# Kernel tuning notes

Measured on AMD Instinct MI355X. Metric: run time of the kernel, lower is better.

Reference implementation:

```python
import jax, jax.numpy as jnp
import numpy as np

D_STATE = 16
DT_RANK = 6
EPS = 1e-5


def layer_norm(x, w, b):
    mu = jnp.mean(x, axis=-1, keepdims=True)
    var = jnp.mean((x - mu) ** 2, axis=-1, keepdims=True)
    return (x - mu) * jax.lax.rsqrt(var + EPS) * w + b


def selective_scan(u, delta, A, Bp, Cp, Dp):
    # u, delta: [B,L,D]; A: [D,N]; Bp, Cp: [B,L,N]; Dp: [D]
    delta_A = jnp.exp(jnp.einsum('bld,dn->bldn', delta, A))          # [B,L,D,N]
    delta_B_u = jnp.einsum('bld,bln,bld->bldn', delta, Bp, u)        # [B,L,D,N]
    Bsz, L, D = u.shape

    def step(x, inp):
        dA_t, dBu_t, C_t = inp                                       # [B,D,N],[B,D,N],[B,N]
        x = dA_t * x + dBu_t
        y = jnp.einsum('bdn,bn->bd', x, C_t)
        return x, y

    x0 = jnp.zeros((Bsz, D, D_STATE), dtype=u.dtype)
    xs = (jnp.swapaxes(delta_A, 0, 1), jnp.swapaxes(delta_B_u, 0, 1), jnp.swapaxes(Cp, 0, 1))
    _, ys = jax.lax.scan(step, x0, xs)                               # ys: [L,B,D]
    y = jnp.swapaxes(ys, 0, 1)
    return y + u * Dp


def ssm(x, x_proj_W, dt_proj_W, dt_proj_b, A_log, D_param):
    A = -jnp.exp(A_log.astype(jnp.float32))                         # [D,N]
    dbc = x @ x_proj_W.T                                             # [B,L,dt_rank+2N]
    delta_r = dbc[..., :DT_RANK]
    Bp = dbc[..., DT_RANK:DT_RANK + D_STATE]
    Cp = dbc[..., DT_RANK + D_STATE:]
    delta = jax.nn.softplus(delta_r @ dt_proj_W.T + dt_proj_b) * 0.001
    return selective_scan(x, delta, A, Bp, Cp, D_param.astype(jnp.float32))


def reference(feat_patch, ln_w, ln_b, in_proj_W, conv_w, conv_b,
              x_proj_W, dt_proj_W, dt_proj_b, A_log, D_param, out_proj_W):
    residual = feat_patch
    x = layer_norm(feat_patch, ln_w, ln_b)
    x = x @ in_proj_W.T                                              # [B,L,96]
    x_ncl = jnp.swapaxes(x, 1, 2)                                    # [B,96,L]
    x_ncl = jax.lax.conv_general_dilated(
        x_ncl, conv_w, window_strides=(1,), padding=((1, 1),),
        dimension_numbers=('NCH', 'OIH', 'NCH'), feature_group_count=96)
    x_ncl = x_ncl + conv_b[None, :, None]
    x = jnp.swapaxes(x_ncl, 1, 2)                                    # [B,L,96]
    x = jax.nn.silu(x)
    y = ssm(x, x_proj_W, dt_proj_W, dt_proj_b, A_log, D_param)
    out = y @ out_proj_W.T                                           # [B,L,2048]
    return out + residual


def setup_inputs() -> dict:
    key = jax.random.key(0)
    ks = jax.random.split(key, 10)
    B, L, C, Din = 16, 2048, 2048, 96
    A = jnp.tile(jnp.arange(1, D_STATE + 1, dtype=jnp.float32)[None, :], (Din, 1))
    return {
        'feat_patch': jax.random.normal(ks[0], (B, L, C), dtype=jnp.float32),
        'ln_w': jnp.ones((C,), jnp.float32),
        'ln_b': jnp.zeros((C,), jnp.float32),
        'in_proj_W': jax.random.normal(ks[1], (Din, C), jnp.float32) * (1.0 / np.sqrt(C)),
        'conv_w': jax.random.normal(ks[2], (Din, 1, 3), jnp.float32) * 0.3,
        'conv_b': jnp.zeros((Din,), jnp.float32),
        'x_proj_W': jax.random.normal(ks[3], (DT_RANK + 2 * D_STATE, Din), jnp.float32) * (1.0 / np.sqrt(Din)),
        'dt_proj_W': jax.random.normal(ks[4], (Din, DT_RANK), jnp.float32) * (1.0 / np.sqrt(DT_RANK)),
        'dt_proj_b': jnp.zeros((Din,), jnp.float32),
        'A_log': jnp.log(A),
        'D_param': jnp.ones((Din,), jnp.float32),
        'out_proj_W': jax.random.normal(ks[5], (C, Din), jnp.float32) * (1.0 / np.sqrt(Din)),
    }
```

## Files before the change

### kernel.cpp

```cpp
#include <hip/hip_runtime.h>
#include <hip/hip_bf16.h>

#define BSZ 16
#define LEN 2048
#define CH  2048
#define DIN 96
#define NST 16
#define RNK 6
#define NROW (BSZ*LEN)
#define TCH  128
#define NCHK (LEN/TCH)
#define NPAIR (BSZ*DIN)

typedef __attribute__((ext_vector_type(4))) float f32x4;
typedef __attribute__((ext_vector_type(8))) short bf16x8;

static __device__ __forceinline__ unsigned short f2bf(float f) {
  union { float f; unsigned u; } v; v.f = f;
  unsigned r = v.u + 0x7fff + ((v.u >> 16) & 1);
  return (unsigned short)(r >> 16);
}

static __device__ __forceinline__ f32x4 mfma16(bf16x8 a, bf16x8 b, f32x4 c) {
  return __builtin_amdgcn_mfma_f32_16x16x32_bf16(a, b, c, 0, 0, 0);
}

__global__ void k_prep(const float* __restrict__ inW, const float* __restrict__ outW,
                       const float* __restrict__ xW, const float* __restrict__ dtW,
                       const float* __restrict__ lnw,
                       unsigned short* __restrict__ inWb, unsigned short* __restrict__ outWb,
                       float* __restrict__ M1t, float* __restrict__ xBC) {
  int i = blockIdx.x * 256 + threadIdx.x;
  if (i < DIN*CH)  inWb[i]  = f2bf(inW[i] * lnw[i & (CH-1)]);
  if (i < CH*DIN)  outWb[i] = f2bf(outW[i]);
  if (i < DIN*DIN) {
    int c = i / DIN, d = i - c*DIN;
    float s = 0.f;
    #pragma unroll
    for (int r = 0; r < RNK; ++r) s += dtW[d*RNK + r] * xW[r*DIN + c];
    M1t[i] = s;
  }
  if (i < DIN*32) {
    int c = i / 32, n = i - c*32;
    xBC[i] = xW[(RNK + n)*DIN + c];
  }
}

__launch_bounds__(256)
__global__ void k_prep2(const float* __restrict__ inW, const float* __restrict__ lnw,
                        const float* __restrict__ lnb,
                        float* __restrict__ pvec, float* __restrict__ qvec) {
  __shared__ float sp_[4], sq_[4];
  const int d = blockIdx.x;
  const int tid = threadIdx.x;
  const float4* w4 = (const float4*)(inW + (size_t)d*CH);
  const float4* a4 = (const float4*)lnw;
  const float4* b4 = (const float4*)lnb;
  float sp = 0.f, sq = 0.f;
  for (int j = tid; j < CH/4; j += 256) {
    float4 w = w4[j], a = a4[j], b = b4[j];
    sp += w.x*a.x + w.y*a.y + w.z*a.z + w.w*a.w;
    sq += w.x*b.x + w.y*b.y + w.z*b.z + w.w*b.w;
  }
  #pragma unroll
  for (int off = 32; off; off >>= 1) { sp += __shfl_xor(sp, off); sq += __shfl_xor(sq, off); }
  if ((tid & 63) == 0) { sp_[tid>>6] = sp; sq_[tid>>6] = sq; }
  __syncthreads();
  if (tid == 0) {
    pvec[d] = sp_[0] + sp_[1] + sp_[2] + sp_[3];
    qvec[d] = sq_[0] + sq_[1] + sq_[2] + sq_[3];
  }
}

#define K2_KC 128
#define K2_WLD 136

__launch_bounds__(512)
__global__ void k_ln_inproj(const float* __restrict__ feat,
                            const unsigned short* __restrict__ Wb,
                            const float* __restrict__ pvec, const float* __restrict__ qvec,
                            float* __restrict__ xin) {
  __shared__ unsigned short W_lds[DIN][K2_WLD];

  const int tid  = threadIdx.x;
  const int lane = tid & 63;
  const int w    = tid >> 6;
  const int wh   = w & 3;
  const int wc   = w >> 2;
  const int r    = lane & 15;
  const int g    = lane >> 4;
  const int row  = blockIdx.x * 64 + wh*16 + r;

  const float* arow = feat + (size_t)row * CH;

  f32x4 acc[3];
  #pragma unroll
  for (int i = 0; i < 3; ++i) acc[i] = (f32x4){0.f, 0.f, 0.f, 0.f};
  float s = 0.f, q = 0.f;

  for (int kc = 0; kc < CH; kc += K2_KC) {
    __syncthreads();
    #pragma unroll
    for (int i = 0; i < 3; ++i) {
      int j = tid + 512*i;
      int wr = j >> 4, c16 = j & 15;
      *(uint4*)&W_lds[wr][c16*8] = *(const uint4*)(Wb + (size_t)wr*CH + kc + c16*8);
    }
    __syncthreads();
    #pragma unroll
    for (int t = 0; t < 4; ++t) {
      const f32x4* ap = (const f32x4*)(arow + kc + t*32 + g*8);
      f32x4 v0 = __builtin_nontemporal_load(ap);
      f32x4 v1 = __builtin_nontemporal_load(ap + 1);
      s += v0[0] + v0[1] + v0[2] + v0[3] + v1[0] + v1[1] + v1[2] + v1[3];
      #pragma unroll
      for (int k = 0; k < 4; ++k) { q = fmaf(v0[k], v0[k], q); q = fmaf(v1[k], v1[k], q); }
      union { bf16x8 v; unsigned short u[8]; } af;
      #pragma unroll
      for (int k = 0; k < 4; ++k) { af.u[k] = f2bf(v0[k]); af.u[4+k] = f2bf(v1[k]); }
      const int krd = t*32 + g*8;
      #pragma unroll
      for (int ct = 0; ct < 3; ++ct) {
        bf16x8 wf = *(const bf16x8*)&W_lds[wc*48 + ct*16 + r][krd];
        acc[ct] = mfma16(wf, af.v, acc[ct]);
      }
    }
  }

  s += __shfl_xor(s, 16); s += __shfl_xor(s, 32);
  q += __shfl_xor(q, 16); q += __shfl_xor(q, 32);
  const float mu = s * (1.f/CH);
  const float rs = rsqrtf(q*(1.f/CH) - mu*mu + 1e-5f);

  float* orow = xin + (size_t)row * DIN;
  #pragma unroll
  for (int ct = 0; ct < 3; ++ct) {
    const int col = wc*48 + ct*16 + g*4;
    float4 pv = *(const float4*)(pvec + col);
    float4 qv = *(const float4*)(qvec + col);
    f32x4 a = acc[ct];
    float4 o;
    o.x = rs*a[0] - rs*mu*pv.x + qv.x;
    o.y = rs*a[1] - rs*mu*pv.y + qv.y;
    o.z = rs*a[2] - rs*mu*pv.z + qv.z;
    o.w = rs*a[3] - rs*mu*pv.w + qv.w;
    *(float4*)(orow + col) = o;
  }
}

#define K3_R 8
__launch_bounds__(128)
__global__ void k_conv_proj(const float* __restrict__ xin,
                            const float* __restrict__ cw, const float* __restrict__ cb,
                            const float* __restrict__ xBC, const float* __restrict__ M1t,
                            const float* __restrict__ dtb,
                            float* __restrict__ ugT, float* __restrict__ dgT,
                            float* __restrict__ Bg, float* __restrict__ Cg) {
  __shared__ float su[K3_R][DIN];
  const int b  = blockIdx.y;
  const int l0 = blockIdx.x * K3_R;
  const int t  = threadIdx.x;

  if (t < DIN) {
    float x[K3_R + 2];
    #pragma unroll
    for (int i = 0; i < K3_R + 2; ++i) {
      int li = l0 - 1 + i;
      x[i] = (li >= 0 && li < LEN) ? xin[((size_t)b*LEN + li)*DIN + t] : 0.f;
    }
    float w0 = cw[t*3], w1 = cw[t*3+1], w2 = cw[t*3+2], bb = cb[t];
    float ua[K3_R];
    #pragma unroll
    for (int r = 0; r < K3_R; ++r) {
      float c = w0*x[r] + w1*x[r+1] + w2*x[r+2] + bb;
      float uu = c / (1.f + __expf(-c));
      su[r][t] = uu;
      ua[r] = uu;
    }
    float* up = ugT + ((size_t)(b*DIN + t))*LEN + l0;
    *(float4*)(up)     = make_float4(ua[0], ua[1], ua[2], ua[3]);
    *(float4*)(up + 4) = make_float4(ua[4], ua[5], ua[6], ua[7]);
  }
  __syncthreads();
  if (t < DIN) {
    float z[K3_R];
    #pragma unroll
    for (int r = 0; r < K3_R; ++r) z[r] = dtb[t];
    for (int c = 0; c < DIN; ++c) {
      float m = M1t[c*DIN + t];
      #pragma unroll
      for (int r = 0; r < K3_R; ++r) z[r] += su[r][c] * m;
    }
    float da[K3_R];
    #pragma unroll
    for (int r = 0; r < K3_R; ++r) {
      float zz = z[r];
      float sp = (zz > 20.f) ? zz : log1pf(__expf(zz));
      da[r] = 0.001f * sp;
    }
    float* dp = dgT + ((size_t)(b*DIN + t))*LEN + l0;
    *(float4*)(dp)     = make_float4(da[0], da[1], da[2], da[3]);
    *(float4*)(dp + 4) = make_float4(da[4], da[5], da[6], da[7]);
  } else if (t < DIN + 32) {
    int n = t - DIN;
    float s[K3_R];
    #pragma unroll
    for (int r = 0; r < K3_R; ++r) s[r] = 0.f;
    for (int c = 0; c < DIN; ++c) {
      float wv = xBC[c*32 + n];
      #pragma unroll
      for (int r = 0; r < K3_R; ++r) s[r] += su[r][c] * wv;
    }
    #pragma unroll
    for (int r = 0; r < K3_R; ++r) {
      size_t row = (size_t)b*LEN + l0 + r;
      if (n < 16) Bg[row*NST + n]        = s[r];
      else        Cg[row*NST + (n - 16)] = s[r];
    }
  }
}

__launch_bounds__(256)
__global__ void k_scan1(const float* __restrict__ dgT, const float* __restrict__ ugT,
                        const float* __restrict__ Bg, const float* __restrict__ Alog,
                        float* __restrict__ carryS, float* __restrict__ carryD) {
  const int tid  = threadIdx.x;
  const int nq   = tid & 3;
  const int pair = blockIdx.x * 64 + (tid >> 2);
  const int chunk = blockIdx.y;
  const int b = pair / DIN, d = pair - b*DIN;
  f32x4 Al = *(const f32x4*)(Alog + d*NST + nq*4);
  f32x4 An4;
  #pragma unroll
  for (int k = 0; k < 4; ++k) An4[k] = -__expf(Al[k]);
  const float* dp  = dgT + ((size_t)(b*DIN + d))*LEN + chunk*TCH;
  const float* up  = ugT + ((size_t)(b*DIN + d))*LEN + chunk*TCH;
  const float* bp_ = Bg + ((size_t)b*LEN + chunk*TCH)*NST + nq*4;

  f32x4 s4 = (f32x4){0.f, 0.f, 0.f, 0.f};
  float sdl = 0.f;
  #pragma unroll 2
  for (int tq = 0; tq < TCH/4; ++tq) {
    f32x4 dl4 = *(const f32x4*)(dp + tq*4);
    f32x4 uu4 = *(const f32x4*)(up + tq*4);
    #pragma unroll
    for (int j = 0; j < 4; ++j) {
      float dl = dl4[j];
      f32x4 bp4 = *(const f32x4*)(bp_ + (size_t)(tq*4 + j)*NST);
      f32x4 dA;
      #pragma unroll
      for (int k = 0; k < 4; ++k) dA[k] = __expf(dl*An4[k]);
      float du = dl * uu4[j];
      s4 = dA*s4 + du*bp4;
      sdl += dl;
    }
  }
  *(f32x4*)(carryS + (size_t)(pair*NCHK + chunk)*16 + nq*4) = s4;
  if (nq == 0) carryD[pair*NCHK + chunk] = sdl;
}

__launch_bounds__(256)
__global__ void k_scan2(const float* __restrict__ carryS, const float* __restrict__ carryD,
                        const float* __restrict__ Alog, float* __restrict__ xstart) {
  const int i = blockIdx.x * 256 + threadIdx.x;
  const int pair = i >> 4, n = i & 15;
  const int d = pair % DIN;
  const float An = -__expf(Alog[d*NST + n]);
  float x = 0.f;
  #pragma unroll
  for (int c = 0; c < NCHK; ++c) {
    xstart[(size_t)(pair*NCHK + c)*16 + n] = x;
    x = fmaf(__expf(An * carryD[pair*NCHK + c]), x, carryS[(size_t)(pair*NCHK + c)*16 + n]);
  }
}

__launch_bounds__(256)
__global__ void k_scan3(const float* __restrict__ dgT, const float* __restrict__ ugT,
                        const float* __restrict__ Bg, const float* __restrict__ Cg,
                        const float* __restrict__ Alog, const float* __restrict__ Dp,
                        const float* __restrict__ xstart, unsigned short* __restrict__ yb) {
  const int tid  = threadIdx.x;
  const int nq   = tid & 3;
  const int pair = blockIdx.x * 64 + (tid >> 2);
  const int chunk = blockIdx.y;
  const int b = pair / DIN, d = pair - b*DIN;
  f32x4 Al = *(const f32x4*)(Alog + d*NST + nq*4);
  f32x4 An4;
  #pragma unroll
  for (int k = 0; k < 4; ++k) An4[k] = -__expf(Al[k]);
  const float Dd = Dp[d];
  const float* dp  = dgT + ((size_t)(b*DIN + d))*LEN + chunk*TCH;
  const float* up  = ugT + ((size_t)(b*DIN + d))*LEN + chunk*TCH;
  const float* bp_ = Bg + ((size_t)b*LEN + chunk*TCH)*NST + nq*4;
  const float* cp_ = Cg + ((size_t)b*LEN + chunk*TCH)*NST + nq*4;
  unsigned short* yp = yb + ((size_t)b*LEN + chunk*TCH)*DIN + d;

  f32x4 s4 = *(const f32x4*)(xstart + (size_t)(pair*NCHK + chunk)*16 + nq*4);
  #pragma unroll 2
  for (int tq = 0; tq < TCH/4; ++tq) {
    f32x4 dl4 = *(const f32x4*)(dp + tq*4);
    f32x4 uu4 = *(const f32x4*)(up + tq*4);
    #pragma unroll
    for (int j = 0; j < 4; ++j) {
      float dl = dl4[j];
      f32x4 bp4 = *(const f32x4*)(bp_ + (size_t)(tq*4 + j)*NST);
      f32x4 cp4 = *(const f32x4*)(cp_ + (size_t)(tq*4 + j)*NST);
      f32x4 dA;
      #pragma unroll
      for (int k = 0; k < 4; ++k) dA[k] = __expf(dl*An4[k]);
      float du = dl * uu4[j];
      s4 = dA*s4 + du*bp4;
      f32x4 pv = s4 * cp4;
      float py = (pv[0] + pv[1]) + (pv[2] + pv[3]);
      py += __shfl_xor(py, 1);
      py += __shfl_xor(py, 2);
      if (nq == 0) yp[(size_t)(tq*4 + j)*DIN] = f2bf(py + uu4[j]*Dd);
    }
  }
}

#define K6_MR 128
#define K6_NC 128
#define K6_LD 104

__launch_bounds__(512)
__global__ void k_outproj(const unsigned short* __restrict__ yb,
                          const unsigned short* __restrict__ Wb,
                          const float* __restrict__ resid,
                          float* __restrict__ out) {
  __shared__ unsigned short W_lds[K6_NC][K6_LD];
  const int tid  = threadIdx.x;
  const int lane = tid & 63;
  const int w    = tid >> 6;
  const int r    = lane & 15;
  const int g    = lane >> 4;
  const int r0   = blockIdx.y * K6_MR;
  const int c0   = blockIdx.x * K6_NC;

  #pragma unroll
  for (int i = 0; i < 3; ++i) {
    int j = tid + 512*i;
    int row = j / 12, c8 = j - row*12;
    *(uint4*)&W_lds[row][c8*8] = *(const uint4*)(Wb + (size_t)(c0 + row)*DIN + c8*8);
  }
  __syncthreads();

  f32x4 acc[8];
  #pragma unroll
  for (int i = 0; i < 8; ++i) acc[i] = (f32x4){0.f, 0.f, 0.f, 0.f};

  const unsigned short* yrow = yb + (size_t)(r0 + w*16 + r)*DIN;
  #pragma unroll
  for (int kt = 0; kt < 3; ++kt) {
    const int krd = kt*32 + g*8;
    bf16x8 y0 = *(const bf16x8*)(yrow + krd);
    #pragma unroll
    for (int ci = 0; ci < 8; ++ci) {
      bf16x8 wf = *(const bf16x8*)&W_lds[ci*16 + r][krd];
      acc[ci] = mfma16(wf, y0, acc[ci]);
    }
  }

  const size_t row = (size_t)(r0 + w*16 + r);
  #pragma unroll
  for (int ci = 0; ci < 8; ++ci) {
    size_t col = (size_t)(c0 + ci*16 + g*4);
    const f32x4 rv = __builtin_nontemporal_load((const f32x4*)(resid + row*CH + col));
    f32x4 o = acc[ci] + rv;
    __builtin_nontemporal_store(o, (f32x4*)(out + row*CH + col));
  }
}

extern "C" void kernel_launch(void* const* d_in, const int* in_sizes, int n_in,
                              void* d_out, int out_size, void* d_ws, size_t ws_size,
                              hipStream_t stream) {
  const float* feat = (const float*)d_in[0];
  const float* lnw  = (const float*)d_in[1];
  const float* lnb  = (const float*)d_in[2];
  const float* inW  = (const float*)d_in[3];
  const float* cw   = (const float*)d_in[4];
  const float* cb   = (const float*)d_in[5];
  const float* xW   = (const float*)d_in[6];
  const float* dtW  = (const float*)d_in[7];
  const float* dtb  = (const float*)d_in[8];
  const float* Alog = (const float*)d_in[9];
  const float* Dp   = (const float*)d_in[10];
  const float* outW = (const float*)d_in[11];
  float* out = (float*)d_out;

  char* ws = (char*)d_ws;
  size_t off = 0;
  auto alloc = [&](size_t bytes) { void* p = ws + off; off += (bytes + 255) & ~255ull; return p; };
  unsigned short* inWb  = (unsigned short*)alloc((size_t)DIN*CH*2);
  unsigned short* outWb = (unsigned short*)alloc((size_t)CH*DIN*2);
  float* M1t = (float*)alloc((size_t)DIN*DIN*4);
  float* xBC = (float*)alloc((size_t)DIN*32*4);
  float* pvec = (float*)alloc((size_t)DIN*4);
  float* qvec = (float*)alloc((size_t)DIN*4);
  float* xin = (float*)alloc((size_t)NROW*DIN*4);
  float* ugT = (float*)alloc((size_t)NROW*DIN*4);
  float* dgT = (float*)alloc((size_t)NROW*DIN*4);
  float* Bg  = (float*)alloc((size_t)NROW*NST*4);
  float* Cg  = (float*)alloc((size_t)NROW*NST*4);
  unsigned short* yb = (unsigned short*)alloc((size_t)NROW*DIN*2);
  float* carryS = (float*)alloc((size_t)NPAIR*NCHK*NST*4);
  float* carryD = (float*)alloc((size_t)NPAIR*NCHK*4);
  float* xstart = (float*)alloc((size_t)NPAIR*NCHK*NST*4);

  hipLaunchKernelGGL(k_prep, dim3((DIN*CH + 255)/256), dim3(256), 0, stream,
                     inW, outW, xW, dtW, lnw, inWb, outWb, M1t, xBC);
  hipLaunchKernelGGL(k_prep2, dim3(DIN), dim3(256), 0, stream,
                     inW, lnw, lnb, pvec, qvec);
  hipLaunchKernelGGL(k_ln_inproj, dim3(NROW/64), dim3(512), 0, stream,
                     feat, inWb, pvec, qvec, xin);
  hipLaunchKernelGGL(k_conv_proj, dim3(LEN/K3_R, BSZ), dim3(128), 0, stream,
                     xin, cw, cb, xBC, M1t, dtb, ugT, dgT, Bg, Cg);
  hipLaunchKernelGGL(k_scan1, dim3(NPAIR/64, NCHK), dim3(256), 0, stream,
                     dgT, ugT, Bg, Alog, carryS, carryD);
  hipLaunchKernelGGL(k_scan2, dim3(NPAIR*NST/256), dim3(256), 0, stream,
                     carryS, carryD, Alog, xstart);
  hipLaunchKernelGGL(k_scan3, dim3(NPAIR/64, NCHK), dim3(256), 0, stream,
                     dgT, ugT, Bg, Cg, Alog, Dp, xstart, yb);
  hipLaunchKernelGGL(k_outproj, dim3(CH/K6_NC, NROW/K6_MR), dim3(512), 0, stream,
                     yb, outWb, feat, out);
}
```

Measured before the change: 357.8 us.

## Pack delta and u as bf16 pairs, fold carry pass into scan3, halve chunks

Delta and the conv output u are now stored as one 32-bit word of two bf16 values instead of two fp32 arrays, which halves the bytes k_conv_proj writes and both scan passes read. The separate k_scan2 carry-propagation kernel is removed. Each k_scan3 block now sums the carries of all earlier chunks itself, trading redundant per-chunk work (quadratic in the chunk count) for one less launch and no xstart round trip. The chunk length drops from 128 to 64, giving more parallel blocks but twice as many carries. Storing delta and u in bf16 lowers the precision of the scan inputs.

```diff
diff --git a/kernel.cpp b/kernel.cpp
--- a/kernel.cpp
+++ b/kernel.cpp
@@ -8,17 +8,23 @@
 #define NST 16
 #define RNK 6
 #define NROW (BSZ*LEN)
-#define TCH  128
+#define TCH  64
 #define NCHK (LEN/TCH)
 #define NPAIR (BSZ*DIN)
 
 typedef __attribute__((ext_vector_type(4))) float f32x4;
+typedef __attribute__((ext_vector_type(4))) unsigned u32x4;
 typedef __attribute__((ext_vector_type(8))) short bf16x8;
 
 static __device__ __forceinline__ unsigned short f2bf(float f) {
   union { float f; unsigned u; } v; v.f = f;
   unsigned r = v.u + 0x7fff + ((v.u >> 16) & 1);
   return (unsigned short)(r >> 16);
+}
+
+static __device__ __forceinline__ float bf2f(unsigned us) {
+  union { float f; unsigned u; } v; v.u = us << 16;
+  return v.f;
 }
 
 static __device__ __forceinline__ f32x4 mfma16(bf16x8 a, bf16x8 b, f32x4 c) {
@@ -154,13 +160,14 @@
                             const float* __restrict__ cw, const float* __restrict__ cb,
                             const float* __restrict__ xBC, const float* __restrict__ M1t,
                             const float* __restrict__ dtb,
-                            float* __restrict__ ugT, float* __restrict__ dgT,
+                            unsigned* __restrict__ duT,
                             float* __restrict__ Bg, float* __restrict__ Cg) {
   __shared__ float su[K3_R][DIN];
   const int b  = blockIdx.y;
   const int l0 = blockIdx.x * K3_R;
   const int t  = threadIdx.x;
 
+  float ua[K3_R];
   if (t < DIN) {
     float x[K3_R + 2];
     #pragma unroll
@@ -169,7 +176,6 @@
       x[i] = (li >= 0 && li < LEN) ? xin[((size_t)b*LEN + li)*DIN + t] : 0.f;
     }
     float w0 = cw[t*3], w1 = cw[t*3+1], w2 = cw[t*3+2], bb = cb[t];
-    float ua[K3_R];
     #pragma unroll
     for (int r = 0; r < K3_R; ++r) {
       float c = w0*x[r] + w1*x[r+1] + w2*x[r+2] + bb;
@@ -177,9 +183,6 @@
       su[r][t] = uu;
       ua[r] = uu;
     }
-    float* up = ugT + ((size_t)(b*DIN + t))*LEN + l0;
-    *(float4*)(up)     = make_float4(ua[0], ua[1], ua[2], ua[3]);
-    *(float4*)(up + 4) = make_float4(ua[4], ua[5], ua[6], ua[7]);
   }
   __syncthreads();
   if (t < DIN) {
@@ -191,16 +194,17 @@
       #pragma unroll
       for (int r = 0; r < K3_R; ++r) z[r] += su[r][c] * m;
     }
-    float da[K3_R];
+    unsigned du[K3_R];
     #pragma unroll
     for (int r = 0; r < K3_R; ++r) {
       float zz = z[r];
       float sp = (zz > 20.f) ? zz : log1pf(__expf(zz));
-      da[r] = 0.001f * sp;
-    }
-    float* dp = dgT + ((size_t)(b*DIN + t))*LEN + l0;
-    *(float4*)(dp)     = make_float4(da[0], da[1], da[2], da[3]);
-    *(float4*)(dp + 4) = make_float4(da[4], da[5], da[6], da[7]);
+      float da = 0.001f * sp;
+      du[r] = (unsigned)f2bf(da) | ((unsigned)f2bf(ua[r]) << 16);
+    }
+    unsigned* dp = duT + ((size_t)(b*DIN + t))*LEN + l0;
+    *(uint4*)(dp)     = make_uint4(du[0], du[1], du[2], du[3]);
+    *(uint4*)(dp + 4) = make_uint4(du[4], du[5], du[6], du[7]);
   } else if (t < DIN + 32) {
     int n = t - DIN;
     float s[K3_R];
@@ -221,7 +225,7 @@
 }
 
 __launch_bounds__(256)
-__global__ void k_scan1(const float* __restrict__ dgT, const float* __restrict__ ugT,
+__global__ void k_scan1(const unsigned* __restrict__ duT,
                         const float* __restrict__ Bg, const float* __restrict__ Alog,
                         float* __restrict__ carryS, float* __restrict__ carryD) {
   const int tid  = threadIdx.x;
@@ -233,24 +237,24 @@
   f32x4 An4;
   #pragma unroll
   for (int k = 0; k < 4; ++k) An4[k] = -__expf(Al[k]);
-  const float* dp  = dgT + ((size_t)(b*DIN + d))*LEN + chunk*TCH;
-  const float* up  = ugT + ((size_t)(b*DIN + d))*LEN + chunk*TCH;
+  const unsigned* dup = duT + ((size_t)(b*DIN + d))*LEN + chunk*TCH;
   const float* bp_ = Bg + ((size_t)b*LEN + chunk*TCH)*NST + nq*4;
 
   f32x4 s4 = (f32x4){0.f, 0.f, 0.f, 0.f};
   float sdl = 0.f;
   #pragma unroll 2
   for (int tq = 0; tq < TCH/4; ++tq) {
-    f32x4 dl4 = *(const f32x4*)(dp + tq*4);
-    f32x4 uu4 = *(const f32x4*)(up + tq*4);
+    u32x4 du4 = *(const u32x4*)(dup + tq*4);
     #pragma unroll
     for (int j = 0; j < 4; ++j) {
-      float dl = dl4[j];
+      unsigned pk = du4[j];
+      float dl = bf2f(pk & 0xffffu);
+      float uu = bf2f(pk >> 16);
       f32x4 bp4 = *(const f32x4*)(bp_ + (size_t)(tq*4 + j)*NST);
       f32x4 dA;
       #pragma unroll
       for (int k = 0; k < 4; ++k) dA[k] = __expf(dl*An4[k]);
-      float du = dl * uu4[j];
+      float du = dl * uu;
       s4 = dA*s4 + du*bp4;
       sdl += dl;
     }
@@ -260,25 +264,11 @@
 }
 
 __launch_bounds__(256)
-__global__ void k_scan2(const float* __restrict__ carryS, const float* __restrict__ carryD,
-                        const float* __restrict__ Alog, float* __restrict__ xstart) {
-  const int i = blockIdx.x * 256 + threadIdx.x;
-  const int pair = i >> 4, n = i & 15;
-  const int d = pair % DIN;
-  const float An = -__expf(Alog[d*NST + n]);
-  float x = 0.f;
-  #pragma unroll
-  for (int c = 0; c < NCHK; ++c) {
-    xstart[(size_t)(pair*NCHK + c)*16 + n] = x;
-    x = fmaf(__expf(An * carryD[pair*NCHK + c]), x, carryS[(size_t)(pair*NCHK + c)*16 + n]);
-  }
-}
-
-__launch_bounds__(256)
-__global__ void k_scan3(const float* __restrict__ dgT, const float* __restrict__ ugT,
+__global__ void k_scan3(const unsigned* __restrict__ duT,
                         const float* __restrict__ Bg, const float* __restrict__ Cg,
                         const float* __restrict__ Alog, const float* __restrict__ Dp,
-                        const float* __restrict__ xstart, unsigned short* __restrict__ yb) {
+                        const float* __restrict__ carryS, const float* __restrict__ carryD,
+                        unsigned short* __restrict__ yb) {
   const int tid  = threadIdx.x;
   const int nq   = tid & 3;
   const int pair = blockIdx.x * 64 + (tid >> 2);
@@ -289,32 +279,42 @@
   #pragma unroll
   for (int k = 0; k < 4; ++k) An4[k] = -__expf(Al[k]);
   const float Dd = Dp[d];
-  const float* dp  = dgT + ((size_t)(b*DIN + d))*LEN + chunk*TCH;
-  const float* up  = ugT + ((size_t)(b*DIN + d))*LEN + chunk*TCH;
+
+  f32x4 s4 = (f32x4){0.f, 0.f, 0.f, 0.f};
+  for (int c = 0; c < chunk; ++c) {
+    float cd = carryD[pair*NCHK + c];
+    f32x4 cs = *(const f32x4*)(carryS + (size_t)(pair*NCHK + c)*16 + nq*4);
+    f32x4 dA;
+    #pragma unroll
+    for (int k = 0; k < 4; ++k) dA[k] = __expf(An4[k] * cd);
+    s4 = dA*s4 + cs;
+  }
+
+  const unsigned* dup = duT + ((size_t)(b*DIN + d))*LEN + chunk*TCH;
   const float* bp_ = Bg + ((size_t)b*LEN + chunk*TCH)*NST + nq*4;
   const float* cp_ = Cg + ((size_t)b*LEN + chunk*TCH)*NST + nq*4;
   unsigned short* yp = yb + ((size_t)b*LEN + chunk*TCH)*DIN + d;
 
-  f32x4 s4 = *(const f32x4*)(xstart + (size_t)(pair*NCHK + chunk)*16 + nq*4);
   #pragma unroll 2
   for (int tq = 0; tq < TCH/4; ++tq) {
-    f32x4 dl4 = *(const f32x4*)(dp + tq*4);
-    f32x4 uu4 = *(const f32x4*)(up + tq*4);
+    u32x4 du4 = *(const u32x4*)(dup + tq*4);
     #pragma unroll
     for (int j = 0; j < 4; ++j) {
-      float dl = dl4[j];
+      unsigned pk = du4[j];
+      float dl = bf2f(pk & 0xffffu);
+      float uu = bf2f(pk >> 16);
       f32x4 bp4 = *(const f32x4*)(bp_ + (size_t)(tq*4 + j)*NST);
       f32x4 cp4 = *(const f32x4*)(cp_ + (size_t)(tq*4 + j)*NST);
       f32x4 dA;
       #pragma unroll
       for (int k = 0; k < 4; ++k) dA[k] = __expf(dl*An4[k]);
-      float du = dl * uu4[j];
+      float du = dl * uu;
       s4 = dA*s4 + du*bp4;
       f32x4 pv = s4 * cp4;
       float py = (pv[0] + pv[1]) + (pv[2] + pv[3]);
       py += __shfl_xor(py, 1);
       py += __shfl_xor(py, 2);
-      if (nq == 0) yp[(size_t)(tq*4 + j)*DIN] = f2bf(py + uu4[j]*Dd);
+      if (nq == 0) yp[(size_t)(tq*4 + j)*DIN] = f2bf(py + uu*Dd);
     }
   }
 }
@@ -398,14 +398,12 @@
   float* pvec = (float*)alloc((size_t)DIN*4);
   float* qvec = (float*)alloc((size_t)DIN*4);
   float* xin = (float*)alloc((size_t)NROW*DIN*4);
-  float* ugT = (float*)alloc((size_t)NROW*DIN*4);
-  float* dgT = (float*)alloc((size_t)NROW*DIN*4);
+  unsigned* duT = (unsigned*)alloc((size_t)NROW*DIN*4);
   float* Bg  = (float*)alloc((size_t)NROW*NST*4);
   float* Cg  = (float*)alloc((size_t)NROW*NST*4);
   unsigned short* yb = (unsigned short*)alloc((size_t)NROW*DIN*2);
   float* carryS = (float*)alloc((size_t)NPAIR*NCHK*NST*4);
   float* carryD = (float*)alloc((size_t)NPAIR*NCHK*4);
-  float* xstart = (float*)alloc((size_t)NPAIR*NCHK*NST*4);
 
   hipLaunchKernelGGL(k_prep, dim3((DIN*CH + 255)/256), dim3(256), 0, stream,
                      inW, outW, xW, dtW, lnw, inWb, outWb, M1t, xBC);
@@ -414,13 +412,11 @@
   hipLaunchKernelGGL(k_ln_inproj, dim3(NROW/64), dim3(512), 0, stream,
                      feat, inWb, pvec, qvec, xin);
   hipLaunchKernelGGL(k_conv_proj, dim3(LEN/K3_R, BSZ), dim3(128), 0, stream,
-                     xin, cw, cb, xBC, M1t, dtb, ugT, dgT, Bg, Cg);
+                     xin, cw, cb, xBC, M1t, dtb, duT, Bg, Cg);
   hipLaunchKernelGGL(k_scan1, dim3(NPAIR/64, NCHK), dim3(256), 0, stream,
-                     dgT, ugT, Bg, Alog, carryS, carryD);
-  hipLaunchKernelGGL(k_scan2, dim3(NPAIR*NST/256), dim3(256), 0, stream,
-                     carryS, carryD, Alog, xstart);
+                     duT, Bg, Alog, carryS, carryD);
   hipLaunchKernelGGL(k_scan3, dim3(NPAIR/64, NCHK), dim3(256), 0, stream,
-                     dgT, ugT, Bg, Cg, Alog, Dp, xstart, yb);
+                     duT, Bg, Cg, Alog, Dp, carryS, carryD, yb);
   hipLaunchKernelGGL(k_outproj, dim3(CH/K6_NC, NROW/K6_MR), dim3(512), 0, stream,
                      yb, outWb, feat, out);
 }
```

New measurement: 346.3 us. -3.2%, faster.
